# Performance work log

Measured on AMD Instinct MI355X. Metric: run time of the kernel, lower is better.

The kernel has to match this reference:

```python
import jax, jax.numpy as jnp
import numpy as np

B, S, H, DH = 2, 2048, 16, 64
DIM = H * DH          # 1024
WIN = 512             # relpos_win_size
LN_EPS = 1e-5


def setup_inputs() -> dict:
    key = jax.random.key(0)
    ks = jax.random.split(key, 8)
    return {
        "q": jax.random.normal(ks[0], (B, S, H, DH), dtype=jnp.float32),
        "k": jax.random.normal(ks[1], (B, S, H, DH), dtype=jnp.float32),
        "relpos_emb": jax.random.normal(ks[2], (WIN, DIM), dtype=jnp.float32),
        "ln_scale": jnp.ones((DIM,), dtype=jnp.float32),
        "ln_bias": jnp.zeros((DIM,), dtype=jnp.float32),
        "Wq": jax.random.normal(ks[3], (DIM, DIM), dtype=jnp.float32),
        "bq": jnp.zeros((DIM,), dtype=jnp.float32),
        "Wk": jax.random.normal(ks[4], (DIM, DIM), dtype=jnp.float32),
        "bk": jnp.zeros((DIM,), dtype=jnp.float32),
    }


def reference(q, k, relpos_emb, ln_scale, ln_bias, Wq, bq, Wk, bk):
    b, nq, h, dh = q.shape
    nk = k.shape[1]
    win = relpos_emb.shape[0]

    # LayerNorm over the embedding dim (use_pos_layer_norm=True); dropout is identity (eval).
    mu = jnp.mean(relpos_emb, axis=-1, keepdims=True)
    var = jnp.mean(jnp.square(relpos_emb - mu), axis=-1, keepdims=True)
    pe = (relpos_emb - mu) * jax.lax.rsqrt(var + LN_EPS) * ln_scale + ln_bias

    qpos = jnp.arange(nq)
    kpos = jnp.arange(nk)
    rel = jnp.clip(kpos[None, :] - qpos[:, None], -(win - 1), 0) + (win - 1)
    idx = jnp.broadcast_to(rel[None, None, :, :], (b, h, nq, nk))

    # Linear projections of the (small) relpos table, split into heads.
    relpos_k = (pe @ Wk.T + bk).reshape(win, h, dh)  # relpos_k_proj
    relpos_q = (pe @ Wq.T + bq).reshape(win, h, dh)  # relpos_q_proj

    # query-to-position: scores over window then gather along window axis (dim 3).
    query_pos_scores = jnp.einsum('bnhx,khx->bhnk', q, relpos_k)
    logits_query_pos = jnp.take_along_axis(query_pos_scores, idx, axis=3)  # [b,h,nq,nk]

    key_pos_scores = jnp.einsum('bnhx,khx->bhkn', k, relpos_q)
    logits_pos_key = jnp.take_along_axis(key_pos_scores, idx, axis=2)      # [b,h,nq,nk]

    # scale_factor = 1 + True + True = 3 (static constant, omitted from array outputs)
    return logits_pos_key, logits_query_pos, relpos_q, relpos_k
```

## Files before the change

### kernel.cpp

```cpp
#include <hip/hip_runtime.h>

#define BB 2
#define S 2048
#define H 16
#define DH 64
#define DIM 1024
#define WIN 512

#define OUT_PK 0
#define OUT_QP 134217728
#define OUT_RQ 268435456
#define OUT_RK 268959744

#define WS_C0Q   1024
#define WS_C511Q (1024 + 65536)
#define WS_C0K   (1024 + 2*65536)
#define WS_C511K (1024 + 3*65536)
#define WS_BF_BASE 263168

typedef short bf16x8 __attribute__((ext_vector_type(8)));
typedef float f32x4 __attribute__((ext_vector_type(4)));

__device__ inline short f2bf(float f) {
    union { float f; unsigned int u; } cv; cv.f = f;
    unsigned int u = cv.u + 0x7FFFu + ((cv.u >> 16) & 1u);
    return (short)(u >> 16);
}

__device__ inline float bf2f(short s) {
    union { unsigned int u; float f; } cv;
    cv.u = ((unsigned int)(unsigned short)s) << 16;
    return cv.f;
}

__global__ __launch_bounds__(256) void proj(const float* __restrict__ emb,
        const float* __restrict__ lnsc, const float* __restrict__ lnbi,
        const float* __restrict__ Wq, const float* __restrict__ bq,
        const float* __restrict__ Wk, const float* __restrict__ bk,
        float* __restrict__ out, short* __restrict__ rqbf, short* __restrict__ rkbf) {
    const float* W    = blockIdx.z ? Wk : Wq;
    const float* bias = blockIdx.z ? bk : bq;
    float* o = out + (blockIdx.z ? OUT_RK : OUT_RQ);
    short* bfo = blockIdx.z ? rkbf : rqbf;
    int r0 = blockIdx.x * 64;
    int d0 = blockIdx.y * 64;
    __shared__ float As[32 * 65];
    __shared__ float Bs[32 * 65];
    __shared__ float smu[64];
    __shared__ float srs[64];
    int t = threadIdx.x;
    int tx = t & 15, ty = t >> 4;

    {
        int rr = t >> 2, p = t & 3;
        const float4* rp = reinterpret_cast<const float4*>(emb + (r0 + rr) * DIM + p * 256);
        float s = 0.f, sq = 0.f;
#pragma unroll
        for (int i = 0; i < 64; ++i) {
            float4 v = rp[i];
            s  += v.x + v.y + v.z + v.w;
            sq += v.x * v.x + v.y * v.y + v.z * v.z + v.w * v.w;
        }
        s += __shfl_xor(s, 1); sq += __shfl_xor(sq, 1);
        s += __shfl_xor(s, 2); sq += __shfl_xor(sq, 2);
        if (p == 0) {
            float mu = s / DIM;
            float var = sq / DIM - mu * mu;
            smu[rr] = mu;
            srs[rr] = rsqrtf(var + 1e-5f);
        }
    }
    __syncthreads();

    float acc[4][4] = {};
    for (int c0 = 0; c0 < DIM; c0 += 32) {
#pragma unroll
        for (int i = 0; i < 8; ++i) {
            int idx = t + i * 256;
            int r = idx >> 5, c = idx & 31;
            float raw = emb[(r0 + r) * DIM + c0 + c];
            float v = (raw - smu[r]) * srs[r] * lnsc[c0 + c] + lnbi[c0 + c];
            As[c * 65 + r] = v;
            Bs[c * 65 + r] = W[(d0 + r) * DIM + c0 + c];
        }
        __syncthreads();
#pragma unroll
        for (int c = 0; c < 32; ++c) {
            float a[4], b[4];
#pragma unroll
            for (int i = 0; i < 4; ++i) a[i] = As[c * 65 + ty * 4 + i];
#pragma unroll
            for (int j = 0; j < 4; ++j) b[j] = Bs[c * 65 + tx * 4 + j];
#pragma unroll
            for (int i = 0; i < 4; ++i)
#pragma unroll
                for (int j = 0; j < 4; ++j) acc[i][j] += a[i] * b[j];
        }
        __syncthreads();
    }
#pragma unroll
    for (int i = 0; i < 4; ++i) {
        int row = r0 + ty * 4 + i, col = d0 + tx * 4;
        float4 v = { acc[i][0] + bias[col], acc[i][1] + bias[col + 1],
                     acc[i][2] + bias[col + 2], acc[i][3] + bias[col + 3] };
        *reinterpret_cast<float4*>(o + row * DIM + col) = v;
        short4 s4 = { f2bf(v.x), f2bf(v.y), f2bf(v.z), f2bf(v.w) };
        int hh = col >> 6, cc = col & 63;
        *reinterpret_cast<short4*>(bfo + ((size_t)(hh * 512) + row) * 64 + cc) = s4;
    }
}

__global__ __launch_bounds__(256) void qkprep(const float* __restrict__ q,
        const float* __restrict__ k, const float* __restrict__ out_ro,
        float* __restrict__ ws, short* __restrict__ qbf, short* __restrict__ kbf) {
    int z = blockIdx.z;
    int bh = blockIdx.y; int b = bh >> 4, h = bh & 15;
    int row = blockIdx.x * 64 + (threadIdx.x >> 2);
    int seg = (threadIdx.x & 3) * 16;
    const float* X = z ? k : q;
    const float* T = out_ro + (z ? OUT_RQ : OUT_RK);
    short* dst = z ? kbf : qbf;
    const float4* xp = reinterpret_cast<const float4*>(X + (size_t)((b * S + row) * H + h) * DH + seg);
    const float4* t0 = reinterpret_cast<const float4*>(T + h * DH + seg);
    const float4* t1 = reinterpret_cast<const float4*>(T + 511 * DIM + h * DH + seg);
    float d0 = 0.f, d1 = 0.f;
    short* dbase = dst + ((size_t)bh * 2048 + row) * 64 + seg;
#pragma unroll
    for (int i = 0; i < 4; ++i) {
        float4 x = xp[i], a = t0[i], c = t1[i];
        d0 += x.x * a.x + x.y * a.y + x.z * a.z + x.w * a.w;
        d1 += x.x * c.x + x.y * c.y + x.z * c.z + x.w * c.w;
        short4 o = { f2bf(x.x), f2bf(x.y), f2bf(x.z), f2bf(x.w) };
        *reinterpret_cast<short4*>(dbase + i * 4) = o;
    }
    d0 += __shfl_xor(d0, 1); d0 += __shfl_xor(d0, 2);
    d1 += __shfl_xor(d1, 1); d1 += __shfl_xor(d1, 2);
    if ((threadIdx.x & 3) == 0) {
        int o = bh * S + row;
        if (!z) { ws[WS_C0Q + o] = d0; ws[WS_C511Q + o] = d1; }
        else    { ws[WS_C0K + o] = d0; ws[WS_C511K + o] = d1; }
    }
}

__global__ __launch_bounds__(256) void outk(const short* __restrict__ qbf,
        const short* __restrict__ kbf, const short* __restrict__ rqbf,
        const short* __restrict__ rkbf, const float* __restrict__ ws,
        float* __restrict__ out) {
    __shared__ short Yt[64 * 132];

    int bid = blockIdx.x;
    int wg = (bid & 7) * 8192 + (bid >> 3);
    int PK = wg >> 15;
    int bh = (wg >> 10) & 31; int h = bh & 15;
    int nt = (wg >> 5) & 31, jt = wg & 31;
    int n0 = nt * 64, j0 = jt * 64;
    int jlo = nt > 8 ? nt - 8 : 0;
    int t = threadIdx.x;
    float* obase = out + (PK ? OUT_PK : OUT_QP) + (size_t)bh * S * S;

    if (jt < jlo || jt > nt) {
        int left = jt < jlo;
        const float* cv = ws + (PK ? (left ? WS_C0K : WS_C511K)
                                   : (left ? WS_C0Q : WS_C511Q)) + bh * S;
        int col4 = t & 15, r0w = t >> 4;
        if (PK) {
            f32x4 v = *reinterpret_cast<const f32x4*>(cv + j0 + col4 * 4);
#pragma unroll
            for (int i = 0; i < 4; ++i) {
                int n = n0 + r0w + i * 16;
                __builtin_nontemporal_store(v,
                    reinterpret_cast<f32x4*>(obase + (size_t)n * S + j0 + col4 * 4));
            }
        } else {
#pragma unroll
            for (int i = 0; i < 4; ++i) {
                int n = n0 + r0w + i * 16;
                float vs = cv[n];
                f32x4 v = { vs, vs, vs, vs };
                __builtin_nontemporal_store(v,
                    reinterpret_cast<f32x4*>(obase + (size_t)n * S + j0 + col4 * 4));
            }
        }
        return;
    }

    int rlo = 511 + j0 - (n0 + 63); rlo = rlo < 0 ? 0 : rlo;

    const short* xb = (PK ? kbf : qbf) + ((size_t)bh * 2048 + (PK ? j0 : n0)) * 64;
    const short* tbase = (PK ? rqbf : rkbf) + (size_t)h * 512 * 64;

    int lane = t & 63, w = t >> 6, lr = lane & 15, lg = lane >> 4;
    const short* arow = xb + (w * 16 + lr) * 64 + lg * 8;
    bf16x8 a0 = *reinterpret_cast<const bf16x8*>(arow);
    bf16x8 a1 = *reinterpret_cast<const bf16x8*>(arow + 32);
#pragma unroll
    for (int s = 0; s < 8; ++s) {
        int trow = rlo + s * 16 + lr;
        trow = trow > 511 ? 511 : trow;
        const short* brow = tbase + trow * 64 + lg * 8;
        bf16x8 b0 = *reinterpret_cast<const bf16x8*>(brow);
        bf16x8 b1 = *reinterpret_cast<const bf16x8*>(brow + 32);
        f32x4 acc = {0.f, 0.f, 0.f, 0.f};
        acc = __builtin_amdgcn_mfma_f32_16x16x32_bf16(a0, b0, acc, 0, 0, 0);
        acc = __builtin_amdgcn_mfma_f32_16x16x32_bf16(a1, b1, acc, 0, 0, 0);
#pragma unroll
        for (int reg = 0; reg < 4; ++reg)
            Yt[(w * 16 + lg * 4 + reg) * 132 + s * 16 + lr] = f2bf(acc[reg]);
    }
    __syncthreads();

    int tx = t & 15, ty = t >> 4;
#pragma unroll
    for (int i = 0; i < 4; ++i) {
        int rowi = ty + i * 16;
        int n = n0 + rowi;
        float vv[4];
#pragma unroll
        for (int jj = 0; jj < 4; ++jj) {
            int j = j0 + tx * 4 + jj;
            int rel = 511 + j - n;
            rel = rel < 0 ? 0 : (rel > 511 ? 511 : rel);
            int g = rel - rlo;
            int m = PK ? (tx * 4 + jj) : rowi;
            vv[jj] = bf2f(Yt[m * 132 + g]);
        }
        f32x4 v = { vv[0], vv[1], vv[2], vv[3] };
        __builtin_nontemporal_store(v,
            reinterpret_cast<f32x4*>(obase + (size_t)n * S + j0 + tx * 4));
    }
}

extern "C" void kernel_launch(void* const* d_in, const int* in_sizes, int n_in,
                              void* d_out, int out_size, void* d_ws, size_t ws_size,
                              hipStream_t stream) {
    const float* q    = (const float*)d_in[0];
    const float* k    = (const float*)d_in[1];
    const float* emb  = (const float*)d_in[2];
    const float* lnsc = (const float*)d_in[3];
    const float* lnbi = (const float*)d_in[4];
    const float* Wq   = (const float*)d_in[5];
    const float* bq   = (const float*)d_in[6];
    const float* Wk   = (const float*)d_in[7];
    const float* bk   = (const float*)d_in[8];
    float* out = (float*)d_out;
    float* ws  = (float*)d_ws;

    short* qbf  = (short*)(ws + WS_BF_BASE);
    short* kbf  = qbf + (size_t)4194304;
    short* rqbf = kbf + (size_t)4194304;
    short* rkbf = rqbf + (size_t)524288;

    proj<<<dim3(8, 16, 2), dim3(256), 0, stream>>>(emb, lnsc, lnbi, Wq, bq, Wk, bk, out, rqbf, rkbf);
    qkprep<<<dim3(32, 32, 2), dim3(256), 0, stream>>>(q, k, out, ws, qbf, kbf);
    outk<<<dim3(65536), dim3(256), 0, stream>>>(qbf, kbf, rqbf, rkbf, ws, out);
}
```

Before: 280.6 us.

## Use bf16 MFMA for relpos projection GEMM and batch B-row loads

The LayerNorm+projection kernel switches from an fp32 scalar-FMA shared-memory GEMM to bf16 MFMA 16x16x32. Operands are converted to bf16 while staged in LDS, and the K tile widens to 64. Separately, the logits kernel now issues all eight B-row loads before running the MFMAs, so memory latency can overlap. This lowers the precision of the fp32 relpos_q/relpos_k outputs, which could affect tolerance, and the epilogue now writes scalars instead of float4.

```diff
diff --git a/kernel.cpp b/kernel.cpp
--- a/kernel.cpp
+++ b/kernel.cpp
@@ -44,12 +44,11 @@
     short* bfo = blockIdx.z ? rkbf : rqbf;
     int r0 = blockIdx.x * 64;
     int d0 = blockIdx.y * 64;
-    __shared__ float As[32 * 65];
-    __shared__ float Bs[32 * 65];
+    __shared__ short As[64 * 72];
+    __shared__ short Bs[64 * 72];
     __shared__ float smu[64];
     __shared__ float srs[64];
     int t = threadIdx.x;
-    int tx = t & 15, ty = t >> 4;
 
     {
         int rr = t >> 2, p = t & 3;
@@ -72,41 +71,54 @@
     }
     __syncthreads();
 
-    float acc[4][4] = {};
-    for (int c0 = 0; c0 < DIM; c0 += 32) {
-#pragma unroll
-        for (int i = 0; i < 8; ++i) {
-            int idx = t + i * 256;
-            int r = idx >> 5, c = idx & 31;
-            float raw = emb[(r0 + r) * DIM + c0 + c];
-            float v = (raw - smu[r]) * srs[r] * lnsc[c0 + c] + lnbi[c0 + c];
-            As[c * 65 + r] = v;
-            Bs[c * 65 + r] = W[(d0 + r) * DIM + c0 + c];
+    int lane = t & 63, w = t >> 6, lr = lane & 15, lg = lane >> 4;
+    int srow = t >> 2, seg = (t & 3) * 16;
+    float mu = smu[srow], rs = srs[srow];
+
+    f32x4 acc[4] = {};
+    for (int c0 = 0; c0 < DIM; c0 += 64) {
+        const float4* ep = reinterpret_cast<const float4*>(emb + (size_t)(r0 + srow) * DIM + c0 + seg);
+        const float4* wp = reinterpret_cast<const float4*>(W + (size_t)(d0 + srow) * DIM + c0 + seg);
+        short4* ad = reinterpret_cast<short4*>(&As[srow * 72 + seg]);
+        short4* wd = reinterpret_cast<short4*>(&Bs[srow * 72 + seg]);
+#pragma unroll
+        for (int i = 0; i < 4; ++i) {
+            float4 v = ep[i], wv = wp[i];
+            int cb = c0 + seg + i * 4;
+            float4 sc = *reinterpret_cast<const float4*>(lnsc + cb);
+            float4 bi = *reinterpret_cast<const float4*>(lnbi + cb);
+            short4 a4 = { f2bf((v.x - mu) * rs * sc.x + bi.x),
+                          f2bf((v.y - mu) * rs * sc.y + bi.y),
+                          f2bf((v.z - mu) * rs * sc.z + bi.z),
+                          f2bf((v.w - mu) * rs * sc.w + bi.w) };
+            short4 w4 = { f2bf(wv.x), f2bf(wv.y), f2bf(wv.z), f2bf(wv.w) };
+            ad[i] = a4;
+            wd[i] = w4;
         }
         __syncthreads();
 #pragma unroll
-        for (int c = 0; c < 32; ++c) {
-            float a[4], b[4];
-#pragma unroll
-            for (int i = 0; i < 4; ++i) a[i] = As[c * 65 + ty * 4 + i];
-#pragma unroll
-            for (int j = 0; j < 4; ++j) b[j] = Bs[c * 65 + tx * 4 + j];
-#pragma unroll
-            for (int i = 0; i < 4; ++i)
-#pragma unroll
-                for (int j = 0; j < 4; ++j) acc[i][j] += a[i] * b[j];
+        for (int kk = 0; kk < 2; ++kk) {
+            bf16x8 a = *reinterpret_cast<const bf16x8*>(&As[(w * 16 + lr) * 72 + kk * 32 + lg * 8]);
+#pragma unroll
+            for (int cg = 0; cg < 4; ++cg) {
+                bf16x8 b = *reinterpret_cast<const bf16x8*>(&Bs[(cg * 16 + lr) * 72 + kk * 32 + lg * 8]);
+                acc[cg] = __builtin_amdgcn_mfma_f32_16x16x32_bf16(a, b, acc[cg], 0, 0, 0);
+            }
         }
         __syncthreads();
     }
 #pragma unroll
-    for (int i = 0; i < 4; ++i) {
-        int row = r0 + ty * 4 + i, col = d0 + tx * 4;
-        float4 v = { acc[i][0] + bias[col], acc[i][1] + bias[col + 1],
-                     acc[i][2] + bias[col + 2], acc[i][3] + bias[col + 3] };
-        *reinterpret_cast<float4*>(o + row * DIM + col) = v;
-        short4 s4 = { f2bf(v.x), f2bf(v.y), f2bf(v.z), f2bf(v.w) };
+    for (int cg = 0; cg < 4; ++cg) {
+        int col = d0 + cg * 16 + lr;
+        float bv = bias[col];
         int hh = col >> 6, cc = col & 63;
-        *reinterpret_cast<short4*>(bfo + ((size_t)(hh * 512) + row) * 64 + cc) = s4;
+#pragma unroll
+        for (int reg = 0; reg < 4; ++reg) {
+            int rr = r0 + w * 16 + lg * 4 + reg;
+            float val = acc[cg][reg] + bv;
+            o[(size_t)rr * DIM + col] = val;
+            bfo[((size_t)(hh * 512) + rr) * 64 + cc] = f2bf(val);
+        }
     }
 }
 
@@ -193,16 +205,21 @@
     const short* arow = xb + (w * 16 + lr) * 64 + lg * 8;
     bf16x8 a0 = *reinterpret_cast<const bf16x8*>(arow);
     bf16x8 a1 = *reinterpret_cast<const bf16x8*>(arow + 32);
+
+    bf16x8 b0s[8], b1s[8];
 #pragma unroll
     for (int s = 0; s < 8; ++s) {
         int trow = rlo + s * 16 + lr;
         trow = trow > 511 ? 511 : trow;
         const short* brow = tbase + trow * 64 + lg * 8;
-        bf16x8 b0 = *reinterpret_cast<const bf16x8*>(brow);
-        bf16x8 b1 = *reinterpret_cast<const bf16x8*>(brow + 32);
+        b0s[s] = *reinterpret_cast<const bf16x8*>(brow);
+        b1s[s] = *reinterpret_cast<const bf16x8*>(brow + 32);
+    }
+#pragma unroll
+    for (int s = 0; s < 8; ++s) {
         f32x4 acc = {0.f, 0.f, 0.f, 0.f};
-        acc = __builtin_amdgcn_mfma_f32_16x16x32_bf16(a0, b0, acc, 0, 0, 0);
-        acc = __builtin_amdgcn_mfma_f32_16x16x32_bf16(a1, b1, acc, 0, 0, 0);
+        acc = __builtin_amdgcn_mfma_f32_16x16x32_bf16(a0, b0s[s], acc, 0, 0, 0);
+        acc = __builtin_amdgcn_mfma_f32_16x16x32_bf16(a1, b1s[s], acc, 0, 0, 0);
 #pragma unroll
         for (int reg = 0; reg < 4; ++reg)
             Yt[(w * 16 + lg * 4 + reg) * 132 + s * 16 + lr] = f2bf(acc[reg]);
```

Result: faster. 234.6 us (-16.4%).
